# Kernel tuning notes

Measured on AMD Instinct MI355X. Metric: run time of the kernel, lower is better.

## Reference

```python
import jax, jax.numpy as jnp
import numpy as np

N, E, L, D, H, NC = 50000, 400000, 1024, 256, 4, 2
C = D // H  # per-head dim


def setup_inputs() -> dict:
    key = jax.random.key(0)
    ks = jax.random.split(key, 12)
    s = 1.0 / np.sqrt(L)
    sd = 1.0 / np.sqrt(D)
    return {
        "x": jax.random.normal(ks[0], (N, L), dtype=jnp.float32),
        "edge_index": jax.random.randint(ks[1], (2, E), 0, N, dtype=jnp.int32),
        "label": 1,
        "Wq": jax.random.normal(ks[2], (L, D), dtype=jnp.float32) * s,
        "bq": jnp.zeros((D,), dtype=jnp.float32),
        "Wk": jax.random.normal(ks[3], (L, D), dtype=jnp.float32) * s,
        "bk": jnp.zeros((D,), dtype=jnp.float32),
        "Wv": jax.random.normal(ks[4], (L, D), dtype=jnp.float32) * s,
        "bv": jnp.zeros((D,), dtype=jnp.float32),
        "Wskip": jax.random.normal(ks[5], (L, D), dtype=jnp.float32) * s,
        "bskip": jnp.zeros((D,), dtype=jnp.float32),
        "gate_w": jax.random.normal(ks[6], (D, NC), dtype=jnp.float32) * sd,
        "gate_b": jnp.zeros((NC,), dtype=jnp.float32),
        "pool_w": jax.random.normal(ks[7], (D, D), dtype=jnp.float32) * sd,
        "pool_b": jnp.zeros((D,), dtype=jnp.float32),
    }


def reference(x, edge_index, label, Wq, bq, Wk, bk, Wv, bv, Wskip, bskip,
              gate_w, gate_b, pool_w, pool_b):
    src, dst = edge_index[0], edge_index[1]
    # per-head projections [N, H, C]
    q = (x @ Wq + bq).reshape(N, H, C)
    k = (x @ Wk + bk).reshape(N, H, C)
    v = (x @ Wv + bv).reshape(N, H, C)
    # edge attention scores, softmax over incoming edges per destination node
    s = jnp.einsum('ehc,ehc->eh', q[dst], k[src]) / np.sqrt(C)  # [E, H]
    m = jax.ops.segment_max(s, dst, num_segments=N)             # [N, H]
    ex = jnp.exp(s - m[dst])
    den = jax.ops.segment_sum(ex, dst, num_segments=N)          # [N, H]
    alpha = ex / den[dst]                                       # [E, H]
    agg = jax.ops.segment_sum(alpha[:, :, None] * v[src], dst,
                              num_segments=N).reshape(N, D)
    h = agg + x @ Wskip + bskip                                 # root/skip term
    h = jax.nn.gelu(h, approximate=False)
    # global adaptive attention pooling: per-class softmax over nodes
    scores = h @ gate_w + gate_b                                # [N, NC]
    attn = jax.nn.softmax(scores, axis=0)                       # [N, NC]
    y = jnp.einsum('nc,nd->cd', attn, h @ pool_w + pool_b)      # [NC, D]
    A = attn[:, label]
    return (y, attn, h, A)
```

## Files before the change

kernel.cpp:

```cpp
#include <hip/hip_runtime.h>
#include <stdint.h>

#define N_NODES 50000
#define N_EDGES 400000
#define M_PAD   50048

typedef __attribute__((ext_vector_type(8))) __bf16 bf16x8;
typedef __attribute__((ext_vector_type(4))) float floatx4;

__device__ __forceinline__ unsigned short f2bf(float f) {
    unsigned int u = __float_as_uint(f);
    unsigned int r = (u + 0x7fffu + ((u >> 16) & 1u)) >> 16;
    return (unsigned short)r;
}

__device__ __forceinline__ void gload_lds16(const void* g, void* l) {
    __builtin_amdgcn_global_load_lds((__attribute__((address_space(1))) void*)g,
                                     (__attribute__((address_space(3))) void*)l,
                                     16, 0, 0);
}

__global__ void k_conv_x(const float* __restrict__ x, unsigned short* __restrict__ xb) {
    const int total = M_PAD * 256;
    for (int u = blockIdx.x * blockDim.x + threadIdx.x; u < total; u += gridDim.x * blockDim.x) {
        int row = u >> 8;
        int c4  = u & 255;
        float4 v = make_float4(0.f, 0.f, 0.f, 0.f);
        if (row < N_NODES) v = ((const float4*)x)[(size_t)row * 256 + c4];
        ushort4 o;
        o.x = f2bf(v.x); o.y = f2bf(v.y); o.z = f2bf(v.z); o.w = f2bf(v.w);
        ((ushort4*)xb)[u] = o;
    }
}

__global__ void k_build_w(const float* __restrict__ Wq, const float* __restrict__ Wk,
                          const float* __restrict__ Wv, const float* __restrict__ Ws,
                          const float* __restrict__ bq, const float* __restrict__ bk,
                          const float* __restrict__ bv, const float* __restrict__ bs,
                          unsigned short* __restrict__ WT, float* __restrict__ biascat) {
    int idx = blockIdx.x * blockDim.x + threadIdx.x;
    if (idx < 1024 * 1024) {
        int n = idx >> 10;
        int k = idx & 1023;
        int g = n >> 8, d = n & 255;
        const float* W = (g == 0) ? Wq : (g == 1) ? Wk : (g == 2) ? Wv : Ws;
        WT[idx] = f2bf(W[k * 256 + d]);
    }
    if (idx < 1024) {
        int g = idx >> 8, d = idx & 255;
        const float* B = (g == 0) ? bq : (g == 1) ? bk : (g == 2) ? bv : bs;
        biascat[idx] = B[d];
    }
}

__launch_bounds__(256)
__global__ void k_gemm(const unsigned short* __restrict__ A,
                       const unsigned short* __restrict__ BT,
                       const float* __restrict__ bias,
                       float* __restrict__ Cmat) {
    __shared__ unsigned short As[128 * 32];
    __shared__ unsigned short Bs[128 * 32];

    int wg   = blockIdx.x;
    int xcd  = wg & 7;
    int j    = wg >> 3;
    int xt   = j & 7;
    int ygrp = j >> 3;
    int yt   = ygrp * 8 + xcd;
    if (yt >= 391) return;

    const int row0 = yt * 128;
    const int col0 = xt * 128;

    const int t = threadIdx.x;
    const int w = t >> 6;
    const int l = t & 63;

    const int lr = l >> 2;
    const int lc = (l & 3) * 8;

    const int wr = (w >> 1) * 64;
    const int wc = (w & 1) * 64;
    const int lane15 = l & 15;
    const int quad = l >> 4;

    floatx4 acc[4][4];
#pragma unroll
    for (int i = 0; i < 4; i++)
#pragma unroll
        for (int j2 = 0; j2 < 4; j2++) acc[i][j2] = (floatx4)0.f;

    for (int kk = 0; kk < 1024; kk += 32) {
        __syncthreads();
#pragma unroll
        for (int issue = 0; issue < 2; issue++) {
            int arow = row0 + issue * 64 + w * 16 + lr;
            gload_lds16(A + (size_t)arow * 1024 + kk + lc, As + issue * 2048 + w * 512);
            int brow = col0 + issue * 64 + w * 16 + lr;
            gload_lds16(BT + (size_t)brow * 1024 + kk + lc, Bs + issue * 2048 + w * 512);
        }
        __builtin_amdgcn_s_waitcnt(0x0f70);
        __syncthreads();

        bf16x8 af[4], bfr[4];
#pragma unroll
        for (int i = 0; i < 4; i++) {
            af[i]  = *(const bf16x8*)(As + (wr + i * 16 + lane15) * 32 + quad * 8);
            bfr[i] = *(const bf16x8*)(Bs + (wc + i * 16 + lane15) * 32 + quad * 8);
        }
#pragma unroll
        for (int i = 0; i < 4; i++)
#pragma unroll
            for (int j2 = 0; j2 < 4; j2++)
                acc[i][j2] = __builtin_amdgcn_mfma_f32_16x16x32_bf16(af[i], bfr[j2], acc[i][j2], 0, 0, 0);
    }

#pragma unroll
    for (int i = 0; i < 4; i++) {
#pragma unroll
        for (int j2 = 0; j2 < 4; j2++) {
            int col = col0 + wc + j2 * 16 + lane15;
            float bcol = bias[col];
#pragma unroll
            for (int r = 0; r < 4; r++) {
                int row = row0 + wr + i * 16 + quad * 4 + r;
                Cmat[(size_t)row * 1024 + col] = acc[i][j2][r] + bcol;
            }
        }
    }
}

__global__ void k_hist(const int* __restrict__ ei, int* __restrict__ cnt) {
    int e = blockIdx.x * blockDim.x + threadIdx.x;
    if (e >= N_EDGES) return;
    atomicAdd(&cnt[ei[N_EDGES + e]], 1);
}

__global__ void k_scan(const int* __restrict__ cnt, int* __restrict__ offs) {
    __shared__ int wsums[4];
    const int CH = 196;
    int t = threadIdx.x;
    int beg = t * CH;
    int end = beg + CH; if (end > N_NODES) end = N_NODES;
    int s = 0;
    for (int i = beg; i < end; i++) s += cnt[i];
    int lane = t & 63, w = t >> 6;
    int v = s;
#pragma unroll
    for (int off = 1; off < 64; off <<= 1) {
        int u = __shfl_up(v, off, 64);
        if (lane >= off) v += u;
    }
    if (lane == 63) wsums[w] = v;
    __syncthreads();
    int carry = 0;
    for (int i = 0; i < w; i++) carry += wsums[i];
    int run = carry + v - s;
    for (int i = beg; i < end; i++) {
        offs[i] = run;
        run += cnt[i];
    }
    if (t == 255) offs[N_NODES] = run;
}

__global__ void k_scatter(const int* __restrict__ ei, const int* __restrict__ offs,
                          int* __restrict__ fill, int* __restrict__ ssrc) {
    int e = blockIdx.x * blockDim.x + threadIdx.x;
    if (e >= N_EDGES) return;
    int src = ei[e];
    int dst = ei[N_EDGES + e];
    int pos = offs[dst] + atomicAdd(&fill[dst], 1);
    ssrc[pos] = src;
}

__launch_bounds__(256)
__global__ void k_attn(const int* __restrict__ offs, const int* __restrict__ ssrc,
                       const float* __restrict__ qkvs,
                       const float* __restrict__ gate_w, const float* __restrict__ gate_b,
                       float* __restrict__ out_h, float* __restrict__ exsc) {
    int w = threadIdx.x >> 6, l = threadIdx.x & 63;
    int n = blockIdx.x * 4 + w;
    if (n >= N_NODES) return;

    float4 qv = ((const float4*)(qkvs + (size_t)n * 1024))[l];
    int beg = offs[n], end = offs[n + 1];

    float4 acc = make_float4(0.f, 0.f, 0.f, 0.f);
    float den = 0.f;

    for (int base = beg; base < end; base += 64) {
        int m = end - base; if (m > 64) m = 64;
        int mysrc = (l < m) ? ssrc[base + l] : 0;
#pragma unroll 2
        for (int j = 0; j < m; j++) {
            int src = __shfl(mysrc, j, 64);
            const float* row = qkvs + (size_t)src * 1024;
            float4 kv = ((const float4*)(row + 256))[l];
            float4 vv = ((const float4*)(row + 512))[l];
            float p = qv.x * kv.x + qv.y * kv.y + qv.z * kv.z + qv.w * kv.w;
            p += __shfl_xor(p, 1, 16);
            p += __shfl_xor(p, 2, 16);
            p += __shfl_xor(p, 4, 16);
            p += __shfl_xor(p, 8, 16);
            float ex = expf(p * 0.125f);
            den += ex;
            acc.x += ex * vv.x; acc.y += ex * vv.y;
            acc.z += ex * vv.z; acc.w += ex * vv.w;
        }
    }

    float inv = (den > 0.f) ? 1.f / den : 0.f;
    float4 sk = ((const float4*)(qkvs + (size_t)n * 1024 + 768))[l];

    float z0 = acc.x * inv + sk.x;
    float z1 = acc.y * inv + sk.y;
    float z2 = acc.z * inv + sk.z;
    float z3 = acc.w * inv + sk.w;

    const float is2 = 0.70710678118f;
    float h0 = 0.5f * z0 * (1.f + erff(z0 * is2));
    float h1 = 0.5f * z1 * (1.f + erff(z1 * is2));
    float h2 = 0.5f * z2 * (1.f + erff(z2 * is2));
    float h3 = 0.5f * z3 * (1.f + erff(z3 * is2));
    ((float4*)(out_h + (size_t)n * 256))[l] = make_float4(h0, h1, h2, h3);

    int d0 = l * 4;
    float s0 = h0 * gate_w[(d0 + 0) * 2] + h1 * gate_w[(d0 + 1) * 2] +
               h2 * gate_w[(d0 + 2) * 2] + h3 * gate_w[(d0 + 3) * 2];
    float s1 = h0 * gate_w[(d0 + 0) * 2 + 1] + h1 * gate_w[(d0 + 1) * 2 + 1] +
               h2 * gate_w[(d0 + 2) * 2 + 1] + h3 * gate_w[(d0 + 3) * 2 + 1];
#pragma unroll
    for (int off = 1; off < 64; off <<= 1) {
        s0 += __shfl_xor(s0, off, 64);
        s1 += __shfl_xor(s1, off, 64);
    }
    if (l == 0) {
        exsc[n * 2 + 0] = expf(s0 + gate_b[0]);
        exsc[n * 2 + 1] = expf(s1 + gate_b[1]);
    }
}

__global__ void k_esum(const float* __restrict__ exsc, float* __restrict__ esum) {
    __shared__ float red0[4], red1[4];
    float p0 = 0.f, p1 = 0.f;
    for (int n = blockIdx.x * blockDim.x + threadIdx.x; n < N_NODES; n += gridDim.x * blockDim.x) {
        p0 += exsc[n * 2];
        p1 += exsc[n * 2 + 1];
    }
#pragma unroll
    for (int off = 1; off < 64; off <<= 1) {
        p0 += __shfl_xor(p0, off, 64);
        p1 += __shfl_xor(p1, off, 64);
    }
    int w = threadIdx.x >> 6, l = threadIdx.x & 63;
    if (l == 0) { red0[w] = p0; red1[w] = p1; }
    __syncthreads();
    if (threadIdx.x == 0) {
        atomicAdd(&esum[0], red0[0] + red0[1] + red0[2] + red0[3]);
        atomicAdd(&esum[1], red1[0] + red1[1] + red1[2] + red1[3]);
    }
}

__global__ void k_t(const float* __restrict__ exsc, const float* __restrict__ esum,
                    const float* __restrict__ h_f, const int* __restrict__ label_p,
                    float* __restrict__ attn_out, float* __restrict__ A_out,
                    float* __restrict__ t_ws) {
    int d = threadIdx.x;
    float inv0 = 1.f / esum[0], inv1 = 1.f / esum[1];
    int lab = *label_p;
    int n0 = blockIdx.x * 98;
    int n1 = n0 + 98; if (n1 > N_NODES) n1 = N_NODES;
    float t0 = 0.f, t1 = 0.f;
    for (int n = n0; n < n1; n++) {
        float e0 = exsc[n * 2], e1 = exsc[n * 2 + 1];
        float a0 = e0 * inv0, a1 = e1 * inv1;
        float hv = h_f[(size_t)n * 256 + d];
        t0 += a0 * hv;
        t1 += a1 * hv;
        if (d == 0) attn_out[n * 2] = a0;
        else if (d == 1) attn_out[n * 2 + 1] = a1;
        else if (d == 2) A_out[n] = (lab == 0) ? a0 : a1;
    }
    atomicAdd(&t_ws[d], t0);
    atomicAdd(&t_ws[256 + d], t1);
}

__global__ void k_y(const float* __restrict__ t_ws, const float* __restrict__ pool_w,
                    const float* __restrict__ pool_b, float* __restrict__ y_out) {
    int d = threadIdx.x;
    float a0 = pool_b[d], a1 = pool_b[d];
    for (int k = 0; k < 256; k++) {
        float w = pool_w[k * 256 + d];
        a0 += t_ws[k] * w;
        a1 += t_ws[256 + k] * w;
    }
    y_out[d] = a0;
    y_out[256 + d] = a1;
}

extern "C" void kernel_launch(void* const* d_in, const int* in_sizes, int n_in,
                              void* d_out, int out_size, void* d_ws, size_t ws_size,
                              hipStream_t stream) {
    const float* x      = (const float*)d_in[0];
    const int*   ei     = (const int*)d_in[1];
    const int*   label  = (const int*)d_in[2];
    const float* Wq     = (const float*)d_in[3];
    const float* bq     = (const float*)d_in[4];
    const float* Wk     = (const float*)d_in[5];
    const float* bk     = (const float*)d_in[6];
    const float* Wv     = (const float*)d_in[7];
    const float* bv     = (const float*)d_in[8];
    const float* Wskip  = (const float*)d_in[9];
    const float* bskip  = (const float*)d_in[10];
    const float* gate_w = (const float*)d_in[11];
    const float* gate_b = (const float*)d_in[12];
    const float* pool_w = (const float*)d_in[13];
    const float* pool_b = (const float*)d_in[14];

    char* ws = (char*)d_ws;
    size_t off = 0;
    float* qkvs = (float*)(ws + off);                 off += (size_t)M_PAD * 1024 * 4;
    unsigned short* xb = (unsigned short*)(ws + off); off += (size_t)M_PAD * 1024 * 2;
    unsigned short* WT = (unsigned short*)(ws + off); off += (size_t)1024 * 1024 * 2;
    float* biascat = (float*)(ws + off);              off += 1024 * 4;
    int* cnt  = (int*)(ws + off);                     off += (size_t)N_NODES * 4;
    int* fill = (int*)(ws + off);                     off += (size_t)N_NODES * 4;
    int* offs = (int*)(ws + off);                     off += (size_t)(N_NODES + 1) * 4;
    int* ssrc = (int*)(ws + off);                     off += (size_t)N_EDGES * 4;
    float* exsc = (float*)(ws + off);                 off += (size_t)N_NODES * 2 * 4;
    float* esum = (float*)(ws + off);                 off += 2 * 4;
    float* t_ws = (float*)(ws + off);                 off += 512 * 4;

    float* out = (float*)d_out;
    float* y_out    = out;
    float* attn_out = out + 512;
    float* h_out    = out + 100512;
    float* A_out    = out + 12900512;

    hipMemsetAsync(cnt, 0, (size_t)N_NODES * 2 * 4, stream);
    hipMemsetAsync(esum, 0, (2 + 512) * 4, stream);

    k_conv_x<<<4096, 256, 0, stream>>>(x, xb);
    k_build_w<<<4096, 256, 0, stream>>>(Wq, Wk, Wv, Wskip, bq, bk, bv, bskip, WT, biascat);
    k_hist<<<(N_EDGES + 255) / 256, 256, 0, stream>>>(ei, cnt);
    k_scan<<<1, 256, 0, stream>>>(cnt, offs);
    k_scatter<<<(N_EDGES + 255) / 256, 256, 0, stream>>>(ei, offs, fill, ssrc);
    k_gemm<<<3136, 256, 0, stream>>>(xb, WT, biascat, qkvs);
    k_attn<<<12500, 256, 0, stream>>>(offs, ssrc, qkvs, gate_w, gate_b, h_out, exsc);
    k_esum<<<128, 256, 0, stream>>>(exsc, esum);
    k_t<<<512, 256, 0, stream>>>(exsc, esum, h_out, label, attn_out, A_out, t_ws);
    k_y<<<1, 256, 0, stream>>>(t_ws, pool_w, pool_b, y_out);
}
```

Measured before the change: 824.0 us.

## Store K/V in bf16 split buffers, fuse preprocessing kernels and esum into attention

The GEMM epilogue now writes Q and skip to separate fp32 buffers and packs K and V into one interleaved bf16 buffer. This halves the bytes the edge-gather loop reads per source row and shrinks its stride. The x conversion, weight transpose and histogram kernels are merged into one launch, and the exp-sum reduction moves into the attention kernel through per-block atomics. Launches are removed in exchange for bf16 rounding of K/V and more atomics on esum.

```diff
diff --git a/kernel.cpp b/kernel.cpp
--- a/kernel.cpp
+++ b/kernel.cpp
@@ -14,126 +14,51 @@
     return (unsigned short)r;
 }
 
+__device__ __forceinline__ float bf2f(unsigned short u) {
+    return __uint_as_float(((unsigned int)u) << 16);
+}
+
 __device__ __forceinline__ void gload_lds16(const void* g, void* l) {
     __builtin_amdgcn_global_load_lds((__attribute__((address_space(1))) void*)g,
                                      (__attribute__((address_space(3))) void*)l,
                                      16, 0, 0);
 }
 
-__global__ void k_conv_x(const float* __restrict__ x, unsigned short* __restrict__ xb) {
-    const int total = M_PAD * 256;
-    for (int u = blockIdx.x * blockDim.x + threadIdx.x; u < total; u += gridDim.x * blockDim.x) {
-        int row = u >> 8;
-        int c4  = u & 255;
-        float4 v = make_float4(0.f, 0.f, 0.f, 0.f);
-        if (row < N_NODES) v = ((const float4*)x)[(size_t)row * 256 + c4];
-        ushort4 o;
-        o.x = f2bf(v.x); o.y = f2bf(v.y); o.z = f2bf(v.z); o.w = f2bf(v.w);
-        ((ushort4*)xb)[u] = o;
-    }
-}
-
-__global__ void k_build_w(const float* __restrict__ Wq, const float* __restrict__ Wk,
-                          const float* __restrict__ Wv, const float* __restrict__ Ws,
-                          const float* __restrict__ bq, const float* __restrict__ bk,
-                          const float* __restrict__ bv, const float* __restrict__ bs,
-                          unsigned short* __restrict__ WT, float* __restrict__ biascat) {
-    int idx = blockIdx.x * blockDim.x + threadIdx.x;
-    if (idx < 1024 * 1024) {
+__global__ void k_pre(const float* __restrict__ x, unsigned short* __restrict__ xb,
+                      const float* __restrict__ Wq, const float* __restrict__ Wk,
+                      const float* __restrict__ Wv, const float* __restrict__ Ws,
+                      const float* __restrict__ bq, const float* __restrict__ bk,
+                      const float* __restrict__ bv, const float* __restrict__ bs,
+                      unsigned short* __restrict__ WT, float* __restrict__ biascat,
+                      const int* __restrict__ ei, int* __restrict__ cnt) {
+    int bid = blockIdx.x;
+    if (bid < 4096) {
+        const int total = M_PAD * 256;
+        for (int u = bid * 256 + threadIdx.x; u < total; u += 4096 * 256) {
+            int row = u >> 8;
+            int c4  = u & 255;
+            float4 v = make_float4(0.f, 0.f, 0.f, 0.f);
+            if (row < N_NODES) v = ((const float4*)x)[(size_t)row * 256 + c4];
+            ushort4 o;
+            o.x = f2bf(v.x); o.y = f2bf(v.y); o.z = f2bf(v.z); o.w = f2bf(v.w);
+            ((ushort4*)xb)[u] = o;
+        }
+    } else if (bid < 8192) {
+        int idx = (bid - 4096) * 256 + threadIdx.x;
         int n = idx >> 10;
         int k = idx & 1023;
         int g = n >> 8, d = n & 255;
         const float* W = (g == 0) ? Wq : (g == 1) ? Wk : (g == 2) ? Wv : Ws;
         WT[idx] = f2bf(W[k * 256 + d]);
-    }
-    if (idx < 1024) {
-        int g = idx >> 8, d = idx & 255;
-        const float* B = (g == 0) ? bq : (g == 1) ? bk : (g == 2) ? bv : bs;
-        biascat[idx] = B[d];
-    }
-}
-
-__launch_bounds__(256)
-__global__ void k_gemm(const unsigned short* __restrict__ A,
-                       const unsigned short* __restrict__ BT,
-                       const float* __restrict__ bias,
-                       float* __restrict__ Cmat) {
-    __shared__ unsigned short As[128 * 32];
-    __shared__ unsigned short Bs[128 * 32];
-
-    int wg   = blockIdx.x;
-    int xcd  = wg & 7;
-    int j    = wg >> 3;
-    int xt   = j & 7;
-    int ygrp = j >> 3;
-    int yt   = ygrp * 8 + xcd;
-    if (yt >= 391) return;
-
-    const int row0 = yt * 128;
-    const int col0 = xt * 128;
-
-    const int t = threadIdx.x;
-    const int w = t >> 6;
-    const int l = t & 63;
-
-    const int lr = l >> 2;
-    const int lc = (l & 3) * 8;
-
-    const int wr = (w >> 1) * 64;
-    const int wc = (w & 1) * 64;
-    const int lane15 = l & 15;
-    const int quad = l >> 4;
-
-    floatx4 acc[4][4];
-#pragma unroll
-    for (int i = 0; i < 4; i++)
-#pragma unroll
-        for (int j2 = 0; j2 < 4; j2++) acc[i][j2] = (floatx4)0.f;
-
-    for (int kk = 0; kk < 1024; kk += 32) {
-        __syncthreads();
-#pragma unroll
-        for (int issue = 0; issue < 2; issue++) {
-            int arow = row0 + issue * 64 + w * 16 + lr;
-            gload_lds16(A + (size_t)arow * 1024 + kk + lc, As + issue * 2048 + w * 512);
-            int brow = col0 + issue * 64 + w * 16 + lr;
-            gload_lds16(BT + (size_t)brow * 1024 + kk + lc, Bs + issue * 2048 + w * 512);
-        }
-        __builtin_amdgcn_s_waitcnt(0x0f70);
-        __syncthreads();
-
-        bf16x8 af[4], bfr[4];
-#pragma unroll
-        for (int i = 0; i < 4; i++) {
-            af[i]  = *(const bf16x8*)(As + (wr + i * 16 + lane15) * 32 + quad * 8);
-            bfr[i] = *(const bf16x8*)(Bs + (wc + i * 16 + lane15) * 32 + quad * 8);
-        }
-#pragma unroll
-        for (int i = 0; i < 4; i++)
-#pragma unroll
-            for (int j2 = 0; j2 < 4; j2++)
-                acc[i][j2] = __builtin_amdgcn_mfma_f32_16x16x32_bf16(af[i], bfr[j2], acc[i][j2], 0, 0, 0);
-    }
-
-#pragma unroll
-    for (int i = 0; i < 4; i++) {
-#pragma unroll
-        for (int j2 = 0; j2 < 4; j2++) {
-            int col = col0 + wc + j2 * 16 + lane15;
-            float bcol = bias[col];
-#pragma unroll
-            for (int r = 0; r < 4; r++) {
-                int row = row0 + wr + i * 16 + quad * 4 + r;
-                Cmat[(size_t)row * 1024 + col] = acc[i][j2][r] + bcol;
-            }
-        }
-    }
-}
-
-__global__ void k_hist(const int* __restrict__ ei, int* __restrict__ cnt) {
-    int e = blockIdx.x * blockDim.x + threadIdx.x;
-    if (e >= N_EDGES) return;
-    atomicAdd(&cnt[ei[N_EDGES + e]], 1);
+        if (idx < 1024) {
+            int g2 = idx >> 8, d2 = idx & 255;
+            const float* B = (g2 == 0) ? bq : (g2 == 1) ? bk : (g2 == 2) ? bv : bs;
+            biascat[idx] = B[d2];
+        }
+    } else {
+        int e = (bid - 8192) * 256 + threadIdx.x;
+        if (e < N_EDGES) atomicAdd(&cnt[ei[N_EDGES + e]], 1);
+    }
 }
 
 __global__ void k_scan(const int* __restrict__ cnt, int* __restrict__ offs) {
@@ -174,15 +99,101 @@
 }
 
 __launch_bounds__(256)
+__global__ void k_gemm(const unsigned short* __restrict__ A,
+                       const unsigned short* __restrict__ BT,
+                       const float* __restrict__ bias,
+                       float* __restrict__ qbuf, unsigned short* __restrict__ kvb,
+                       float* __restrict__ sbuf) {
+    __shared__ unsigned short As[128 * 32];
+    __shared__ unsigned short Bs[128 * 32];
+
+    int wg   = blockIdx.x;
+    int xcd  = wg & 7;
+    int j    = wg >> 3;
+    int xt   = j & 7;
+    int ygrp = j >> 3;
+    int yt   = ygrp * 8 + xcd;
+    if (yt >= 391) return;
+
+    const int row0 = yt * 128;
+    const int col0 = xt * 128;
+
+    const int t = threadIdx.x;
+    const int w = t >> 6;
+    const int l = t & 63;
+
+    const int lr = l >> 2;
+    const int lc = (l & 3) * 8;
+
+    const int wr = (w >> 1) * 64;
+    const int wc = (w & 1) * 64;
+    const int lane15 = l & 15;
+    const int quad = l >> 4;
+
+    floatx4 acc[4][4];
+#pragma unroll
+    for (int i = 0; i < 4; i++)
+#pragma unroll
+        for (int j2 = 0; j2 < 4; j2++) acc[i][j2] = (floatx4)0.f;
+
+    for (int kk = 0; kk < 1024; kk += 32) {
+        __syncthreads();
+#pragma unroll
+        for (int issue = 0; issue < 2; issue++) {
+            int arow = row0 + issue * 64 + w * 16 + lr;
+            gload_lds16(A + (size_t)arow * 1024 + kk + lc, As + issue * 2048 + w * 512);
+            int brow = col0 + issue * 64 + w * 16 + lr;
+            gload_lds16(BT + (size_t)brow * 1024 + kk + lc, Bs + issue * 2048 + w * 512);
+        }
+        __builtin_amdgcn_s_waitcnt(0x0f70);
+        __syncthreads();
+
+        bf16x8 af[4], bfr[4];
+#pragma unroll
+        for (int i = 0; i < 4; i++) {
+            af[i]  = *(const bf16x8*)(As + (wr + i * 16 + lane15) * 32 + quad * 8);
+            bfr[i] = *(const bf16x8*)(Bs + (wc + i * 16 + lane15) * 32 + quad * 8);
+        }
+#pragma unroll
+        for (int i = 0; i < 4; i++)
+#pragma unroll
+            for (int j2 = 0; j2 < 4; j2++)
+                acc[i][j2] = __builtin_amdgcn_mfma_f32_16x16x32_bf16(af[i], bfr[j2], acc[i][j2], 0, 0, 0);
+    }
+
+#pragma unroll
+    for (int i = 0; i < 4; i++) {
+#pragma unroll
+        for (int j2 = 0; j2 < 4; j2++) {
+            int col = col0 + wc + j2 * 16 + lane15;
+            int g = col >> 8;
+            int d = col & 255;
+            float bcol = bias[col];
+#pragma unroll
+            for (int r = 0; r < 4; r++) {
+                int row = row0 + wr + i * 16 + quad * 4 + r;
+                float val = acc[i][j2][r] + bcol;
+                if (g == 0)      qbuf[(size_t)row * 256 + d] = val;
+                else if (g == 1) kvb[(size_t)row * 512 + d] = f2bf(val);
+                else if (g == 2) kvb[(size_t)row * 512 + 256 + d] = f2bf(val);
+                else             sbuf[(size_t)row * 256 + d] = val;
+            }
+        }
+    }
+}
+
+__launch_bounds__(256)
 __global__ void k_attn(const int* __restrict__ offs, const int* __restrict__ ssrc,
-                       const float* __restrict__ qkvs,
+                       const float* __restrict__ qbuf, const unsigned short* __restrict__ kvb,
+                       const float* __restrict__ sbuf,
                        const float* __restrict__ gate_w, const float* __restrict__ gate_b,
-                       float* __restrict__ out_h, float* __restrict__ exsc) {
+                       float* __restrict__ out_h, float* __restrict__ exsc,
+                       float* __restrict__ esum) {
+    __shared__ float se0[4], se1[4];
     int w = threadIdx.x >> 6, l = threadIdx.x & 63;
     int n = blockIdx.x * 4 + w;
-    if (n >= N_NODES) return;
-
-    float4 qv = ((const float4*)(qkvs + (size_t)n * 1024))[l];
+
+    float4 qv = ((const float4*)(qbuf + (size_t)n * 256))[l];
     int beg = offs[n], end = offs[n + 1];
 
     float4 acc = make_float4(0.f, 0.f, 0.f, 0.f);
@@ -194,23 +205,24 @@
 #pragma unroll 2
         for (int j = 0; j < m; j++) {
             int src = __shfl(mysrc, j, 64);
-            const float* row = qkvs + (size_t)src * 1024;
-            float4 kv = ((const float4*)(row + 256))[l];
-            float4 vv = ((const float4*)(row + 512))[l];
-            float p = qv.x * kv.x + qv.y * kv.y + qv.z * kv.z + qv.w * kv.w;
+            const unsigned short* row = kvb + (size_t)src * 512;
+            ushort4 ku = ((const ushort4*)row)[l];
+            ushort4 vu = ((const ushort4*)(row + 256))[l];
+            float p = qv.x * bf2f(ku.x) + qv.y * bf2f(ku.y) +
+                      qv.z * bf2f(ku.z) + qv.w * bf2f(ku.w);
             p += __shfl_xor(p, 1, 16);
             p += __shfl_xor(p, 2, 16);
             p += __shfl_xor(p, 4, 16);
             p += __shfl_xor(p, 8, 16);
             float ex = expf(p * 0.125f);
             den += ex;
-            acc.x += ex * vv.x; acc.y += ex * vv.y;
-            acc.z += ex * vv.z; acc.w += ex * vv.w;
+            acc.x += ex * bf2f(vu.x); acc.y += ex * bf2f(vu.y);
+            acc.z += ex * bf2f(vu.z); acc.w += ex * bf2f(vu.w);
         }
     }
 
     float inv = (den > 0.f) ? 1.f / den : 0.f;
-    float4 sk = ((const float4*)(qkvs + (size_t)n * 1024 + 768))[l];
+    float4 sk = ((const float4*)(sbuf + (size_t)n * 256))[l];
 
     float z0 = acc.x * inv + sk.x;
     float z1 = acc.y * inv + sk.y;
@@ -234,30 +246,18 @@
         s0 += __shfl_xor(s0, off, 64);
         s1 += __shfl_xor(s1, off, 64);
     }
+    float e0 = 0.f, e1 = 0.f;
     if (l == 0) {
-        exsc[n * 2 + 0] = expf(s0 + gate_b[0]);
-        exsc[n * 2 + 1] = expf(s1 + gate_b[1]);
-    }
-}
-
-__global__ void k_esum(const float* __restrict__ exsc, float* __restrict__ esum) {
-    __shared__ float red0[4], red1[4];
-    float p0 = 0.f, p1 = 0.f;
-    for (int n = blockIdx.x * blockDim.x + threadIdx.x; n < N_NODES; n += gridDim.x * blockDim.x) {
-        p0 += exsc[n * 2];
-        p1 += exsc[n * 2 + 1];
-    }
-#pragma unroll
-    for (int off = 1; off < 64; off <<= 1) {
-        p0 += __shfl_xor(p0, off, 64);
-        p1 += __shfl_xor(p1, off, 64);
-    }
-    int w = threadIdx.x >> 6, l = threadIdx.x & 63;
-    if (l == 0) { red0[w] = p0; red1[w] = p1; }
+        e0 = expf(s0 + gate_b[0]);
+        e1 = expf(s1 + gate_b[1]);
+        exsc[n * 2 + 0] = e0;
+        exsc[n * 2 + 1] = e1;
+        se0[w] = e0; se1[w] = e1;
+    }
     __syncthreads();
     if (threadIdx.x == 0) {
-        atomicAdd(&esum[0], red0[0] + red0[1] + red0[2] + red0[3]);
-        atomicAdd(&esum[1], red1[0] + red1[1] + red1[2] + red1[3]);
+        atomicAdd(&esum[0], se0[0] + se0[1] + se0[2] + se0[3]);
+        atomicAdd(&esum[1], se1[0] + se1[1] + se1[2] + se1[3]);
     }
 }
 
@@ -319,7 +319,9 @@
 
     char* ws = (char*)d_ws;
     size_t off = 0;
-    float* qkvs = (float*)(ws + off);                 off += (size_t)M_PAD * 1024 * 4;
+    float* qbuf = (float*)(ws + off);                 off += (size_t)M_PAD * 256 * 4;
+    unsigned short* kvb = (unsigned short*)(ws + off);off += (size_t)M_PAD * 512 * 2;
+    float* sbuf = (float*)(ws + off);                 off += (size_t)M_PAD * 256 * 4;
     unsigned short* xb = (unsigned short*)(ws + off); off += (size_t)M_PAD * 1024 * 2;
     unsigned short* WT = (unsigned short*)(ws + off); off += (size_t)1024 * 1024 * 2;
     float* biascat = (float*)(ws + off);              off += 1024 * 4;
@@ -340,14 +342,13 @@
     hipMemsetAsync(cnt, 0, (size_t)N_NODES * 2 * 4, stream);
     hipMemsetAsync(esum, 0, (2 + 512) * 4, stream);
 
-    k_conv_x<<<4096, 256, 0, stream>>>(x, xb);
-    k_build_w<<<4096, 256, 0, stream>>>(Wq, Wk, Wv, Wskip, bq, bk, bv, bskip, WT, biascat);
-    k_hist<<<(N_EDGES + 255) / 256, 256, 0, stream>>>(ei, cnt);
+    k_pre<<<9755, 256, 0, stream>>>(x, xb, Wq, Wk, Wv, Wskip, bq, bk, bv, bskip,
+                                    WT, biascat, ei, cnt);
     k_scan<<<1, 256, 0, stream>>>(cnt, offs);
     k_scatter<<<(N_EDGES + 255) / 256, 256, 0, stream>>>(ei, offs, fill, ssrc);
-    k_gemm<<<3136, 256, 0, stream>>>(xb, WT, biascat, qkvs);
-    k_attn<<<12500, 256, 0, stream>>>(offs, ssrc, qkvs, gate_w, gate_b, h_out, exsc);
-    k_esum<<<128, 256, 0, stream>>>(exsc, esum);
+    k_gemm<<<3136, 256, 0, stream>>>(xb, WT, biascat, qbuf, kvb, sbuf);
+    k_attn<<<12500, 256, 0, stream>>>(offs, ssrc, qbuf, kvb, sbuf, gate_w, gate_b,
+                                      h_out, exsc, esum);
     k_t<<<512, 256, 0, stream>>>(exsc, esum, h_out, label, attn_out, A_out, t_ws);
     k_y<<<1, 256, 0, stream>>>(t_ws, pool_w, pool_b, y_out);
 }
```

New measurement: 1.012 ms. +22.9%, slower.
